# Kernel optimization log

Hardware: AMD Instinct MI355X
Metric: run time of the kernel (lower is better)

## Reference

```python
import jax, jax.numpy as jnp
import numpy as np

B, N, C, H = 4, 4096, 128, 4


def setup_inputs() -> dict:
    key = jax.random.key(0)
    ks = jax.random.split(key, 12)
    def rn(k, shape, s=0.02):
        return jax.random.normal(k, shape, jnp.float32) * s
    return dict(
        x=jax.random.normal(ks[0], (B, N, C), jnp.float32),
        p=jax.random.normal(ks[1], (B, N, 3), jnp.float32),
        fcl1_w=rn(ks[2], (C, C)), fcl1_b=jnp.zeros((C,), jnp.float32),
        # per-head (stacked over leading H axis) TransformerLayer params
        hq_w=rn(ks[3], (H, C, C)), hq_b=jnp.zeros((H, C), jnp.float32),
        hk_w=rn(ks[4], (H, C, C)), hk_b=jnp.zeros((H, C), jnp.float32),
        hv_w=rn(ks[5], (H, C, C)), hv_b=jnp.zeros((H, C), jnp.float32),
        pe1_w=rn(ks[6], (H, C, 3)), pe1_b=jnp.zeros((H, C), jnp.float32),  # Conv1d(3->C, k=1)
        pe2_w=rn(ks[7], (H, C, C)), pe2_b=jnp.zeros((H, C), jnp.float32),  # Conv1d(C->C, k=1)
        mh_w=rn(ks[8], (C, 4 * C)), mh_b=jnp.zeros((C,), jnp.float32),
        fcl2_w=rn(ks[9], (C, C)), fcl2_b=jnp.zeros((C,), jnp.float32),
    )


def reference(x, p, fcl1_w, fcl1_b, hq_w, hq_b, hk_w, hk_b, hv_w, hv_b,
              pe1_w, pe1_b, pe2_w, pe2_b, mh_w, mh_b, fcl2_w, fcl2_b):
    residual = x
    xf = x @ fcl1_w.T + fcl1_b  # fcl1
    scale = 1.0 / jnp.sqrt(jnp.asarray(C, jnp.float32))

    def head(qw, qb, kw, kb, vw, vb, p1w, p1b, p2w, p2b):
        # kernel-size-1 Conv1d == pointwise linear over coords
        pe = jax.nn.relu(jnp.einsum('bnd,cd->bnc', p, p1w) + p1b)
        pe = jnp.einsum('bnc,dc->bnd', pe, p2w) + p2b
        xh = xf + pe
        q = xh @ kw.T + kb  # note: original uses self.key for x_query
        k = xh @ qw.T + qb  # and self.query for x_key (name swap, kept faithful)
        v = xh @ vw.T + vb
        s = jax.nn.softmax(jnp.einsum('bnc,bmc->bnm', q, k) * scale, axis=-1)
        return jnp.einsum('bnm,bmc->bnc', s, v)

    outs = jax.vmap(head)(hq_w, hq_b, hk_w, hk_b, hv_w, hv_b,
                          pe1_w, pe1_b, pe2_w, pe2_b)  # [H,B,N,C]
    cat = jnp.moveaxis(outs, 0, 2).reshape(B, N, H * C)  # concat head1..head4 on last dim
    y = cat @ mh_w.T + mh_b
    y = y @ fcl2_w.T + fcl2_b
    mu = jnp.mean(y, axis=-1, keepdims=True)
    var = jnp.var(y, axis=-1, keepdims=True)
    y = (y - mu) / jnp.sqrt(var + 1e-5)  # torch.layer_norm, no affine
    return (y + residual, p)
```

## Files before the change

### kernel.cpp

```cpp
#include <hip/hip_runtime.h>
#include <hip/hip_bf16.h>

typedef __bf16 bf16;
typedef bf16 bf16x8 __attribute__((ext_vector_type(8)));
typedef float f32x4 __attribute__((ext_vector_type(4)));

static __device__ __forceinline__ f32x4 mfma16(bf16x8 a, bf16x8 b, f32x4 c) {
  return __builtin_amdgcn_mfma_f32_16x16x32_bf16(a, b, c, 0, 0, 0);
}

typedef __attribute__((address_space(3))) void lds_t;
typedef const __attribute__((address_space(1))) void gm_t;

#define N_SEG 18
#define TOTAL_CONV 2511616

struct ConvArgs { const void* src[N_SEG]; };

__global__ __launch_bounds__(256) void convall_k(ConvArgs a, bf16* __restrict__ dst,
                                                 void* __restrict__ outp,
                                                 int* __restrict__ flag) {
  const int ends[N_SEG] = {2097152, 2146304, 2162688, 2162816, 2228352, 2228864,
                           2294400, 2294912, 2360448, 2360960, 2362496, 2363008,
                           2428544, 2429056, 2494592, 2495104, 2511488, 2511616};
  const unsigned short* xr = (const unsigned short*)a.src[0];
  int wild = 0;
#pragma unroll
  for (int j = 0; j < 2; j++) {
    unsigned short w = xr[threadIdx.x * 2 + j];
    int e = (w >> 7) & 0xFF;
    if (e < 110 || e > 134) wild++;
  }
#pragma unroll
  for (int off = 1; off < 64; off <<= 1) wild += __shfl_xor(wild, off);
  __shared__ int red[4];
  if ((threadIdx.x & 63) == 0) red[threadIdx.x >> 6] = wild;
  __syncthreads();
  const int isF32 = (red[0] + red[1] + red[2] + red[3]) > 64;
  if (blockIdx.x == 0 && threadIdx.x == 0) *flag = isF32;

  int i = blockIdx.x * 256 + threadIdx.x;
  if (i >= TOTAL_CONV) {
    int j = i - TOTAL_CONV;
    if (j < 49152) {
      if (isF32) ((float*)outp)[2097152 + j] = ((const float*)a.src[1])[j];
      else       ((bf16*)outp)[2097152 + j]  = ((const bf16*)a.src[1])[j];
    }
    return;
  }
  int s = 0;
  while (i >= ends[s]) s++;
  int j = i - (s ? ends[s - 1] : 0);
  if (isF32) dst[i] = (bf16)((const float*)a.src[s])[j];
  else       dst[i] = ((const bf16*)a.src[s])[j];
}

__global__ __launch_bounds__(256, 2) void pre_k(
    const bf16* __restrict__ x, const bf16* __restrict__ p,
    const bf16* __restrict__ f1w, const bf16* __restrict__ f1b,
    const bf16* __restrict__ pe1w, const bf16* __restrict__ pe1b,
    const bf16* __restrict__ pe2w, const bf16* __restrict__ pe2b,
    const bf16* __restrict__ Wq, const bf16* __restrict__ Bq,
    const bf16* __restrict__ Wk, const bf16* __restrict__ Bk,
    const bf16* __restrict__ Wv, const bf16* __restrict__ Bv,
    bf16* __restrict__ qo, bf16* __restrict__ ko, bf16* __restrict__ vo)
{
  const int lane = threadIdx.x & 63;
  const int wave = threadIdx.x >> 6;
  const int quad = lane >> 4;
  const int n15 = lane & 15;
  const int h = blockIdx.y;
  const int r0 = blockIdx.x * 64;
  const int wr = wave * 16;

  __shared__ bf16 tile[9216];

  f32x4 acc[8];
  const f32x4 zz = {};

  {
    bf16x8 ap = {};
    if (quad == 0) {
      const bf16* pr = p + (long)(r0 + wr + n15) * 3;
      ap[0] = pr[0]; ap[1] = pr[1]; ap[2] = pr[2];
    }
#pragma unroll
    for (int ct = 0; ct < 8; ct++) {
      bf16x8 bw = {};
      if (quad == 0) {
        const bf16* wp = pe1w + ((long)h * 128 + ct * 16 + n15) * 3;
        bw[0] = wp[0]; bw[1] = wp[1]; bw[2] = wp[2];
      }
      acc[ct] = mfma16(ap, bw, zz);
    }
#pragma unroll
    for (int ct = 0; ct < 8; ct++) {
      const int col = ct * 16 + n15;
      const float bb = (float)pe1b[h * 128 + col];
#pragma unroll
      for (int r = 0; r < 4; r++)
        tile[(wr + quad * 4 + r) * 136 + col] = (bf16)fmaxf(acc[ct][r] + bb, 0.f);
    }
  }

#pragma unroll
  for (int ct = 0; ct < 8; ct++) acc[ct] = zz;
#pragma unroll
  for (int kk = 0; kk < 4; kk++) {
    const int ka = kk * 32 + quad * 8;
    bf16x8 a0 = *(const bf16x8*)&tile[(wr + n15) * 136 + ka];
#pragma unroll
    for (int ct = 0; ct < 8; ct++) {
      bf16x8 wf = *(const bf16x8*)(pe2w + (long)h * 16384 + (long)(ct * 16 + n15) * 128 + ka);
      acc[ct] = mfma16(a0, wf, acc[ct]);
    }
  }
#pragma unroll
  for (int kk = 0; kk < 4; kk++) {
    const int ka = kk * 32 + quad * 8;
    bf16x8 a0 = *(const bf16x8*)(x + (long)(r0 + wr + n15) * 128 + ka);
#pragma unroll
    for (int ct = 0; ct < 8; ct++) {
      bf16x8 wf = *(const bf16x8*)(f1w + (long)(ct * 16 + n15) * 128 + ka);
      acc[ct] = mfma16(a0, wf, acc[ct]);
    }
  }
#pragma unroll
  for (int ct = 0; ct < 8; ct++) {
    const int col = ct * 16 + n15;
    const float bv = (float)pe2b[h * 128 + col] + (float)f1b[col];
#pragma unroll
    for (int r = 0; r < 4; r++)
      tile[(wr + quad * 4 + r) * 136 + col] = (bf16)(acc[ct][r] + bv);
  }

  bf16x8 af[4];
#pragma unroll
  for (int kk = 0; kk < 4; kk++)
    af[kk] = *(const bf16x8*)&tile[(wr + n15) * 136 + kk * 32 + quad * 8];

#pragma unroll
  for (int m = 0; m < 2; m++) {
    f32x4 a2[8];
#pragma unroll
    for (int ct = 0; ct < 8; ct++) a2[ct] = zz;
    const bf16* Wm = (m == 0) ? Wq : Wk;
#pragma unroll
    for (int kk = 0; kk < 4; kk++) {
      const int ka = kk * 32 + quad * 8;
#pragma unroll
      for (int ct = 0; ct < 8; ct++) {
        bf16x8 wf = *(const bf16x8*)(Wm + (long)h * 16384 + (long)(ct * 16 + n15) * 128 + ka);
        a2[ct] = mfma16(af[kk], wf, a2[ct]);
      }
    }
    bf16* oz = ((m == 0) ? qo : ko) + (long)h * 2097152;
    const bf16* Bz = (m == 0) ? Bq : Bk;
    const float sc = (m == 0) ? 0.12751743f : 1.0f;
#pragma unroll
    for (int ct = 0; ct < 8; ct++) {
      const int col = ct * 16 + n15;
      const float bv = (float)Bz[h * 128 + col];
#pragma unroll
      for (int r = 0; r < 4; r++)
        oz[(long)(r0 + wr + quad * 4 + r) * 128 + col] = (bf16)((a2[ct][r] + bv) * sc);
    }
  }

  {
    f32x4 a2[8];
#pragma unroll
    for (int ct = 0; ct < 8; ct++) a2[ct] = zz;
#pragma unroll
    for (int kk = 0; kk < 4; kk++) {
      const int ka = kk * 32 + quad * 8;
#pragma unroll
      for (int ct = 0; ct < 8; ct++) {
        bf16x8 wf = *(const bf16x8*)(Wv + (long)h * 16384 + (long)(ct * 16 + n15) * 128 + ka);
        a2[ct] = mfma16(af[kk], wf, a2[ct]);
      }
    }
    __syncthreads();
#pragma unroll
    for (int ct = 0; ct < 8; ct++) {
      const int col = ct * 16 + n15;
      const float bv = (float)Bv[h * 128 + col];
#pragma unroll
      for (int r = 0; r < 4; r++)
        tile[col * 72 + (wr + quad * 4 + r)] = (bf16)(a2[ct][r] + bv);
    }
    __syncthreads();
    bf16* vz = vo + (long)h * 2097152;
#pragma unroll
    for (int i = 0; i < 16; i++) {
      const int c = wave * 32 + i * 2 + (lane >> 5);
      const int m2 = (lane & 31) * 2;
      *(unsigned int*)&vz[(long)c * 16384 + r0 + m2] =
          *(const unsigned int*)&tile[c * 72 + m2];
    }
  }
}

__global__ __launch_bounds__(256, 2) void attn_k(
    const bf16* __restrict__ Q, const bf16* __restrict__ Kg,
    const bf16* __restrict__ vT, bf16* __restrict__ cat)
{
  const int lane = threadIdx.x & 63;
  const int wave = threadIdx.x >> 6;
  const int quad = lane >> 4;
  const int n15 = lane & 15;
  const int b = blockIdx.y, h = blockIdx.z;
  const long qkBase = ((long)h * 4 + b) * 4096 * 128;
  const long vBase = (long)h * (128L * 16384) + (long)b * 4096;
  const int wrow = blockIdx.x * 128 + wave * 32;

  __shared__ bf16 Kt[2][64 * 128];
  __shared__ bf16 Vt[2][128 * 64];
  __shared__ bf16 Pt[8][1024];

  bf16x8 qf[2][4];
#pragma unroll
  for (int g = 0; g < 2; g++)
#pragma unroll
    for (int kk = 0; kk < 4; kk++)
      qf[g][kk] = *(const bf16x8*)(Q + qkBase + (long)(wrow + g * 16 + n15) * 128 + kk * 32 + quad * 8);

  const int krl  = lane >> 4;
  const int kpch = lane & 15;
  const int vcl  = lane >> 3;
  const int vpch = lane & 7;

  f32x4 Om[2][8] = {};
  float l_part[2][4] = {};

#pragma unroll
  for (int i = 0; i < 4; i++) {
    const int row = wave * 16 + i * 4 + krl;
    const int ch = kpch ^ (row & 15);
    __builtin_amdgcn_global_load_lds(
        (gm_t*)(Kg + qkBase + (long)row * 128 + ch * 8),
        (lds_t*)&Kt[0][(wave * 16 + i * 4) * 128], 16, 0, 0);
  }
#pragma unroll
  for (int i = 0; i < 4; i++) {
    const int c = wave * 32 + i * 8 + vcl;
    const int vch = vpch ^ (c & 7);
    __builtin_amdgcn_global_load_lds(
        (gm_t*)(vT + vBase + (long)c * 16384 + vch * 8),
        (lds_t*)&Vt[0][(wave * 32 + i * 8) * 64], 16, 0, 0);
  }

  for (int it = 0; it < 64; it++) {
    __syncthreads();
    const int cb = it & 1;
    if (it + 1 < 64) {
      const int kv1 = (it + 1) * 64;
      const int nb = cb ^ 1;
#pragma unroll
      for (int i = 0; i < 4; i++) {
        const int row = wave * 16 + i * 4 + krl;
        const int ch = kpch ^ (row & 15);
        __builtin_amdgcn_global_load_lds(
            (gm_t*)(Kg + qkBase + (long)(kv1 + row) * 128 + ch * 8),
            (lds_t*)&Kt[nb][(wave * 16 + i * 4) * 128], 16, 0, 0);
      }
#pragma unroll
      for (int i = 0; i < 4; i++) {
        const int c = wave * 32 + i * 8 + vcl;
        const int vch = vpch ^ (c & 7);
        __builtin_amdgcn_global_load_lds(
            (gm_t*)(vT + vBase + (long)c * 16384 + kv1 + vch * 8),
            (lds_t*)&Vt[nb][(wave * 32 + i * 8) * 64], 16, 0, 0);
      }
    }

    f32x4 S[2][4] = {};
#pragma unroll
    for (int kk = 0; kk < 4; kk++) {
#pragma unroll
      for (int ct = 0; ct < 4; ct++) {
        bf16x8 kf = *(const bf16x8*)&Kt[cb][(ct * 16 + n15) * 128 + (((kk * 4 + quad) ^ n15) * 8)];
        S[0][ct] = mfma16(qf[0][kk], kf, S[0][ct]);
        S[1][ct] = mfma16(qf[1][kk], kf, S[1][ct]);
      }
    }

#pragma unroll
    for (int g = 0; g < 2; g++)
#pragma unroll
      for (int ct = 0; ct < 4; ct++)
#pragma unroll
        for (int r = 0; r < 4; r++) {
          float e = __builtin_amdgcn_exp2f(S[g][ct][r]);
          l_part[g][r] += e;
          const int row = quad * 4 + r;
          const int kv = ct * 16 + n15;
          Pt[wave * 2 + g][row * 64 + ((((kv >> 3) ^ (row & 7)) * 8)) + (kv & 7)] = (bf16)e;
        }

#pragma unroll
    for (int kk = 0; kk < 2; kk++) {
      bf16x8 vf[8];
#pragma unroll
      for (int ct = 0; ct < 8; ct++) {
        const int c = ct * 16 + n15;
        vf[ct] = *(const bf16x8*)&Vt[cb][c * 64 + (((kk * 4 + quad) ^ (c & 7)) * 8)];
      }
#pragma unroll
      for (int g = 0; g < 2; g++) {
        bf16x8 pf = *(const bf16x8*)&Pt[wave * 2 + g][n15 * 64 + (((kk * 4 + quad) ^ (n15 & 7)) * 8)];
#pragma unroll
        for (int ct = 0; ct < 8; ct++)
          Om[g][ct] = mfma16(pf, vf[ct], Om[g][ct]);
      }
    }
  }

#pragma unroll
  for (int g = 0; g < 2; g++) {
    float inv[4];
#pragma unroll
    for (int r = 0; r < 4; r++) {
      float s = l_part[g][r];
#pragma unroll
      for (int off = 1; off < 16; off <<= 1) s += __shfl_xor(s, off);
      inv[r] = 1.f / s;
    }
    const long ob = ((long)b * 4096 + wrow + g * 16 + quad * 4) * 512 + h * 128;
#pragma unroll
    for (int ct = 0; ct < 8; ct++)
#pragma unroll
      for (int r = 0; r < 4; r++)
        cat[ob + (long)r * 512 + ct * 16 + n15] = (bf16)(Om[g][ct][r] * inv[r]);
  }
}

__global__ __launch_bounds__(256) void tail_k(
    const bf16* __restrict__ cat,
    const bf16* __restrict__ mhw, const bf16* __restrict__ mhb,
    const bf16* __restrict__ f2w, const bf16* __restrict__ f2b,
    const void* __restrict__ xraw, void* __restrict__ outraw,
    const int* __restrict__ flag)
{
  const int lane = threadIdx.x & 63;
  const int wave = threadIdx.x >> 6;
  const int quad = lane >> 4;
  const int n15 = lane & 15;
  const int r0 = blockIdx.x * 64 + wave * 16;
  __shared__ bf16 y1t[64][136];

  f32x4 acc[8] = {};
  for (int k0 = 0; k0 < 512; k0 += 32) {
    const int ka = k0 + quad * 8;
    bf16x8 a0 = *(const bf16x8*)(cat + (long)(r0 + n15) * 512 + ka);
#pragma unroll
    for (int ct = 0; ct < 8; ct++) {
      bf16x8 wf = *(const bf16x8*)(mhw + (long)(ct * 16 + n15) * 512 + ka);
      acc[ct] = mfma16(a0, wf, acc[ct]);
    }
  }
#pragma unroll
  for (int ct = 0; ct < 8; ct++) {
    const float bv = (float)mhb[ct * 16 + n15];
#pragma unroll
    for (int r = 0; r < 4; r++)
      y1t[wave * 16 + quad * 4 + r][ct * 16 + n15] = (bf16)(acc[ct][r] + bv);
  }

  f32x4 acc2[8] = {};
  for (int k0 = 0; k0 < 128; k0 += 32) {
    const int ka = k0 + quad * 8;
    bf16x8 a0 = *(const bf16x8*)&y1t[wave * 16 + n15][ka];
#pragma unroll
    for (int ct = 0; ct < 8; ct++) {
      bf16x8 wf = *(const bf16x8*)(f2w + (long)(ct * 16 + n15) * 128 + ka);
      acc2[ct] = mfma16(a0, wf, acc2[ct]);
    }
  }

  float s1[4] = {}, s2[4] = {};
#pragma unroll
  for (int ct = 0; ct < 8; ct++) {
    const float bv = (float)f2b[ct * 16 + n15];
#pragma unroll
    for (int r = 0; r < 4; r++) {
      const float v = acc2[ct][r] + bv;
      acc2[ct][r] = v;
      s1[r] += v;
      s2[r] += v * v;
    }
  }
  float mu[4], inv[4];
#pragma unroll
  for (int r = 0; r < 4; r++) {
    float a = s1[r], b2 = s2[r];
#pragma unroll
    for (int off = 1; off < 16; off <<= 1) {
      a += __shfl_xor(a, off);
      b2 += __shfl_xor(b2, off);
    }
    mu[r] = a * (1.f / 128.f);
    const float var = fmaxf(b2 * (1.f / 128.f) - mu[r] * mu[r], 0.f);
    inv[r] = rsqrtf(var + 1e-5f);
  }

  const int isF32 = *flag;
#pragma unroll
  for (int ct = 0; ct < 8; ct++)
#pragma unroll
    for (int r = 0; r < 4; r++) {
      const long idx = (long)(r0 + quad * 4 + r) * 128 + ct * 16 + n15;
      const float resid = isF32 ? ((const float*)xraw)[idx]
                                : (float)((const bf16*)xraw)[idx];
      const float v = (acc2[ct][r] - mu[r]) * inv[r] + resid;
      if (isF32) ((float*)outraw)[idx] = v;
      else       ((bf16*)outraw)[idx] = (bf16)v;
    }
}

extern "C" void kernel_launch(void* const* d_in, const int* in_sizes, int n_in,
                              void* d_out, int out_size, void* d_ws, size_t ws_size,
                              hipStream_t stream)
{
  bf16* ws  = (bf16*)d_ws;
  bf16* q   = ws;
  bf16* kb  = ws + 8388608;
  bf16* vt  = ws + 16777216;
  bf16* cat = ws + 25165824;
  const long AR = 33554432;
  int* flag = (int*)(ws + 36066048);

  static const int counts[N_SEG] = {2097152, 49152, 16384, 128, 65536, 512, 65536, 512,
                                    65536, 512, 1536, 512, 65536, 512, 65536, 512, 16384, 128};
  long offs[N_SEG]; long o = AR;
  for (int i = 0; i < N_SEG; i++) { offs[i] = o; o += counts[i]; }
  bf16* xc    = ws + offs[0];
  bf16* pc    = ws + offs[1];
  bf16* f1w   = ws + offs[2];
  bf16* f1b   = ws + offs[3];
  bf16* hqw   = ws + offs[4];
  bf16* hqb   = ws + offs[5];
  bf16* hkw   = ws + offs[6];
  bf16* hkb   = ws + offs[7];
  bf16* hvw   = ws + offs[8];
  bf16* hvb   = ws + offs[9];
  bf16* pe1w  = ws + offs[10];
  bf16* pe1b  = ws + offs[11];
  bf16* pe2w  = ws + offs[12];
  bf16* pe2b  = ws + offs[13];
  bf16* mhw   = ws + offs[14];
  bf16* mhb   = ws + offs[15];
  bf16* f2w   = ws + offs[16];
  bf16* f2b   = ws + offs[17];

  ConvArgs ca;
  for (int i = 0; i < N_SEG; i++) ca.src[i] = d_in[i];
  convall_k<<<dim3((TOTAL_CONV + 49152 + 255) / 256), dim3(256), 0, stream>>>(ca, ws + AR, d_out, flag);

  dim3 blk(256);
  pre_k<<<dim3(256, 4), blk, 0, stream>>>(xc, pc, f1w, f1b, pe1w, pe1b, pe2w, pe2b,
                                          hkw, hkb, hqw, hqb, hvw, hvb, q, kb, vt);
  attn_k<<<dim3(32, 4, 4), blk, 0, stream>>>(q, kb, vt, cat);
  tail_k<<<dim3(256), blk, 0, stream>>>(cat, mhw, mhb, f2w, f2b, d_in[0], d_out, flag);
}
```

Before: 358.2 us.

## Vectorize conversion, double rows per wave in pre_k, split tail_k columns across waves

The conversion kernel now handles 8 elements per thread with vector loads and stores. pre_k gives each wave 32 rows instead of 16, so every weight fragment feeds two MFMAs, and it writes the transposed V with 16-byte stores. tail_k shrinks to 16 rows per 128-thread block, with the two waves splitting the output columns and combining layernorm sums through shared memory, which yields four times as many blocks. The risks are more register pressure in pre_k, fewer pre_k blocks, and an extra barrier in tail_k. Segment boundaries in the conversion must be multiples of 8, which they appear to be.

```diff
diff --git a/kernel.cpp b/kernel.cpp
--- a/kernel.cpp
+++ b/kernel.cpp
@@ -39,20 +39,31 @@
   const int isF32 = (red[0] + red[1] + red[2] + red[3]) > 64;
   if (blockIdx.x == 0 && threadIdx.x == 0) *flag = isF32;
 
-  int i = blockIdx.x * 256 + threadIdx.x;
+  long i = ((long)blockIdx.x * 256 + threadIdx.x) * 8;
   if (i >= TOTAL_CONV) {
-    int j = i - TOTAL_CONV;
+    long j = i - TOTAL_CONV;
     if (j < 49152) {
-      if (isF32) ((float*)outp)[2097152 + j] = ((const float*)a.src[1])[j];
-      else       ((bf16*)outp)[2097152 + j]  = ((const bf16*)a.src[1])[j];
+      if (isF32) {
+#pragma unroll
+        for (int t = 0; t < 8; t++)
+          ((float*)outp)[2097152 + j + t] = ((const float*)a.src[1])[j + t];
+      } else {
+        *(bf16x8*)&((bf16*)outp)[2097152 + j] = *(const bf16x8*)&((const bf16*)a.src[1])[j];
+      }
     }
     return;
   }
   int s = 0;
   while (i >= ends[s]) s++;
-  int j = i - (s ? ends[s - 1] : 0);
-  if (isF32) dst[i] = (bf16)((const float*)a.src[s])[j];
-  else       dst[i] = ((const bf16*)a.src[s])[j];
+  long j = i - (s ? ends[s - 1] : 0);
+  if (isF32) {
+    bf16x8 v;
+#pragma unroll
+    for (int t = 0; t < 8; t++) v[t] = (bf16)((const float*)a.src[s])[j + t];
+    *(bf16x8*)&dst[i] = v;
+  } else {
+    *(bf16x8*)&dst[i] = *(const bf16x8*)&((const bf16*)a.src[s])[j];
+  }
 }
 
 __global__ __launch_bounds__(256, 2) void pre_k(
@@ -70,19 +81,21 @@
   const int quad = lane >> 4;
   const int n15 = lane & 15;
   const int h = blockIdx.y;
-  const int r0 = blockIdx.x * 64;
-  const int wr = wave * 16;
-
-  __shared__ bf16 tile[9216];
-
-  f32x4 acc[8];
+  const int r0 = blockIdx.x * 128;
+  const int wr = wave * 32;
+
+  __shared__ bf16 tile[128 * 136];
+
+  f32x4 acc[2][8];
   const f32x4 zz = {};
 
   {
-    bf16x8 ap = {};
+    bf16x8 ap0 = {}, ap1 = {};
     if (quad == 0) {
-      const bf16* pr = p + (long)(r0 + wr + n15) * 3;
-      ap[0] = pr[0]; ap[1] = pr[1]; ap[2] = pr[2];
+      const bf16* pr0 = p + (long)(r0 + wr + n15) * 3;
+      const bf16* pr1 = p + (long)(r0 + wr + 16 + n15) * 3;
+      ap0[0] = pr0[0]; ap0[1] = pr0[1]; ap0[2] = pr0[2];
+      ap1[0] = pr1[0]; ap1[1] = pr1[1]; ap1[2] = pr1[2];
     }
 #pragma unroll
     for (int ct = 0; ct < 8; ct++) {
@@ -91,59 +104,73 @@
         const bf16* wp = pe1w + ((long)h * 128 + ct * 16 + n15) * 3;
         bw[0] = wp[0]; bw[1] = wp[1]; bw[2] = wp[2];
       }
-      acc[ct] = mfma16(ap, bw, zz);
-    }
-#pragma unroll
-    for (int ct = 0; ct < 8; ct++) {
-      const int col = ct * 16 + n15;
-      const float bb = (float)pe1b[h * 128 + col];
-#pragma unroll
-      for (int r = 0; r < 4; r++)
-        tile[(wr + quad * 4 + r) * 136 + col] = (bf16)fmaxf(acc[ct][r] + bb, 0.f);
-    }
-  }
-
-#pragma unroll
-  for (int ct = 0; ct < 8; ct++) acc[ct] = zz;
+      acc[0][ct] = mfma16(ap0, bw, zz);
+      acc[1][ct] = mfma16(ap1, bw, zz);
+    }
+#pragma unroll
+    for (int g = 0; g < 2; g++)
+#pragma unroll
+      for (int ct = 0; ct < 8; ct++) {
+        const int col = ct * 16 + n15;
+        const float bb = (float)pe1b[h * 128 + col];
+#pragma unroll
+        for (int r = 0; r < 4; r++)
+          tile[(wr + g * 16 + quad * 4 + r) * 136 + col] = (bf16)fmaxf(acc[g][ct][r] + bb, 0.f);
+      }
+  }
+
+#pragma unroll
+  for (int g = 0; g < 2; g++)
+#pragma unroll
+    for (int ct = 0; ct < 8; ct++) acc[g][ct] = zz;
 #pragma unroll
   for (int kk = 0; kk < 4; kk++) {
     const int ka = kk * 32 + quad * 8;
     bf16x8 a0 = *(const bf16x8*)&tile[(wr + n15) * 136 + ka];
+    bf16x8 a1 = *(const bf16x8*)&tile[(wr + 16 + n15) * 136 + ka];
 #pragma unroll
     for (int ct = 0; ct < 8; ct++) {
       bf16x8 wf = *(const bf16x8*)(pe2w + (long)h * 16384 + (long)(ct * 16 + n15) * 128 + ka);
-      acc[ct] = mfma16(a0, wf, acc[ct]);
+      acc[0][ct] = mfma16(a0, wf, acc[0][ct]);
+      acc[1][ct] = mfma16(a1, wf, acc[1][ct]);
     }
   }
 #pragma unroll
   for (int kk = 0; kk < 4; kk++) {
     const int ka = kk * 32 + quad * 8;
     bf16x8 a0 = *(const bf16x8*)(x + (long)(r0 + wr + n15) * 128 + ka);
+    bf16x8 a1 = *(const bf16x8*)(x + (long)(r0 + wr + 16 + n15) * 128 + ka);
 #pragma unroll
     for (int ct = 0; ct < 8; ct++) {
       bf16x8 wf = *(const bf16x8*)(f1w + (long)(ct * 16 + n15) * 128 + ka);
-      acc[ct] = mfma16(a0, wf, acc[ct]);
-    }
-  }
-#pragma unroll
-  for (int ct = 0; ct < 8; ct++) {
-    const int col = ct * 16 + n15;
-    const float bv = (float)pe2b[h * 128 + col] + (float)f1b[col];
-#pragma unroll
-    for (int r = 0; r < 4; r++)
-      tile[(wr + quad * 4 + r) * 136 + col] = (bf16)(acc[ct][r] + bv);
-  }
-
-  bf16x8 af[4];
-#pragma unroll
-  for (int kk = 0; kk < 4; kk++)
-    af[kk] = *(const bf16x8*)&tile[(wr + n15) * 136 + kk * 32 + quad * 8];
+      acc[0][ct] = mfma16(a0, wf, acc[0][ct]);
+      acc[1][ct] = mfma16(a1, wf, acc[1][ct]);
+    }
+  }
+#pragma unroll
+  for (int g = 0; g < 2; g++)
+#pragma unroll
+    for (int ct = 0; ct < 8; ct++) {
+      const int col = ct * 16 + n15;
+      const float bv = (float)pe2b[h * 128 + col] + (float)f1b[col];
+#pragma unroll
+      for (int r = 0; r < 4; r++)
+        tile[(wr + g * 16 + quad * 4 + r) * 136 + col] = (bf16)(acc[g][ct][r] + bv);
+    }
+
+  bf16x8 af[2][4];
+#pragma unroll
+  for (int g = 0; g < 2; g++)
+#pragma unroll
+    for (int kk = 0; kk < 4; kk++)
+      af[g][kk] = *(const bf16x8*)&tile[(wr + g * 16 + n15) * 136 + kk * 32 + quad * 8];
 
 #pragma unroll
   for (int m = 0; m < 2; m++) {
-    f32x4 a2[8];
-#pragma unroll
-    for (int ct = 0; ct < 8; ct++) a2[ct] = zz;
+#pragma unroll
+    for (int g = 0; g < 2; g++)
+#pragma unroll
+      for (int ct = 0; ct < 8; ct++) acc[g][ct] = zz;
     const bf16* Wm = (m == 0) ? Wq : Wk;
 #pragma unroll
     for (int kk = 0; kk < 4; kk++) {
@@ -151,52 +178,59 @@
 #pragma unroll
       for (int ct = 0; ct < 8; ct++) {
         bf16x8 wf = *(const bf16x8*)(Wm + (long)h * 16384 + (long)(ct * 16 + n15) * 128 + ka);
-        a2[ct] = mfma16(af[kk], wf, a2[ct]);
+        acc[0][ct] = mfma16(af[0][kk], wf, acc[0][ct]);
+        acc[1][ct] = mfma16(af[1][kk], wf, acc[1][ct]);
       }
     }
     bf16* oz = ((m == 0) ? qo : ko) + (long)h * 2097152;
     const bf16* Bz = (m == 0) ? Bq : Bk;
     const float sc = (m == 0) ? 0.12751743f : 1.0f;
 #pragma unroll
-    for (int ct = 0; ct < 8; ct++) {
-      const int col = ct * 16 + n15;
-      const float bv = (float)Bz[h * 128 + col];
-#pragma unroll
-      for (int r = 0; r < 4; r++)
-        oz[(long)(r0 + wr + quad * 4 + r) * 128 + col] = (bf16)((a2[ct][r] + bv) * sc);
-    }
+    for (int g = 0; g < 2; g++)
+#pragma unroll
+      for (int ct = 0; ct < 8; ct++) {
+        const int col = ct * 16 + n15;
+        const float bv = (float)Bz[h * 128 + col];
+#pragma unroll
+        for (int r = 0; r < 4; r++)
+          oz[(long)(r0 + wr + g * 16 + quad * 4 + r) * 128 + col] = (bf16)((acc[g][ct][r] + bv) * sc);
+      }
   }
 
   {
-    f32x4 a2[8];
-#pragma unroll
-    for (int ct = 0; ct < 8; ct++) a2[ct] = zz;
+#pragma unroll
+    for (int g = 0; g < 2; g++)
+#pragma unroll
+      for (int ct = 0; ct < 8; ct++) acc[g][ct] = zz;
 #pragma unroll
     for (int kk = 0; kk < 4; kk++) {
       const int ka = kk * 32 + quad * 8;
 #pragma unroll
       for (int ct = 0; ct < 8; ct++) {
         bf16x8 wf = *(const bf16x8*)(Wv + (long)h * 16384 + (long)(ct * 16 + n15) * 128 + ka);
-        a2[ct] = mfma16(af[kk], wf, a2[ct]);
+        acc[0][ct] = mfma16(af[0][kk], wf, acc[0][ct]);
+        acc[1][ct] = mfma16(af[1][kk], wf, acc[1][ct]);
       }
     }
     __syncthreads();
 #pragma unroll
-    for (int ct = 0; ct < 8; ct++) {
-      const int col = ct * 16 + n15;
-      const float bv = (float)Bv[h * 128 + col];
-#pragma unroll
-      for (int r = 0; r < 4; r++)
-        tile[col * 72 + (wr + quad * 4 + r)] = (bf16)(a2[ct][r] + bv);
-    }
+    for (int g = 0; g < 2; g++)
+#pragma unroll
+      for (int ct = 0; ct < 8; ct++) {
+        const int col = ct * 16 + n15;
+        const float bv = (float)Bv[h * 128 + col];
+#pragma unroll
+        for (int r = 0; r < 4; r++)
+          tile[col * 136 + (wr + g * 16 + quad * 4 + r)] = (bf16)(acc[g][ct][r] + bv);
+      }
     __syncthreads();
     bf16* vz = vo + (long)h * 2097152;
-#pragma unroll
-    for (int i = 0; i < 16; i++) {
-      const int c = wave * 32 + i * 2 + (lane >> 5);
-      const int m2 = (lane & 31) * 2;
-      *(unsigned int*)&vz[(long)c * 16384 + r0 + m2] =
-          *(const unsigned int*)&tile[c * 72 + m2];
+    const int mloc = (threadIdx.x & 15) * 8;
+    const int cbase = threadIdx.x >> 4;
+#pragma unroll
+    for (int cc = 0; cc < 8; cc++) {
+      const int c = cc * 16 + cbase;
+      *(bf16x8*)&vz[(long)c * 16384 + r0 + mloc] = *(const bf16x8*)&tile[c * 136 + mloc];
     }
   }
 }
@@ -335,7 +369,7 @@
   }
 }
 
-__global__ __launch_bounds__(256) void tail_k(
+__global__ __launch_bounds__(128) void tail_k(
     const bf16* __restrict__ cat,
     const bf16* __restrict__ mhw, const bf16* __restrict__ mhb,
     const bf16* __restrict__ f2w, const bf16* __restrict__ f2b,
@@ -346,42 +380,45 @@
   const int wave = threadIdx.x >> 6;
   const int quad = lane >> 4;
   const int n15 = lane & 15;
-  const int r0 = blockIdx.x * 64 + wave * 16;
-  __shared__ bf16 y1t[64][136];
-
-  f32x4 acc[8] = {};
+  const int r0 = blockIdx.x * 16;
+  __shared__ bf16 y1t[16][136];
+  __shared__ float lred[2][2][16];
+
+  f32x4 acc[4] = {};
   for (int k0 = 0; k0 < 512; k0 += 32) {
     const int ka = k0 + quad * 8;
     bf16x8 a0 = *(const bf16x8*)(cat + (long)(r0 + n15) * 512 + ka);
 #pragma unroll
-    for (int ct = 0; ct < 8; ct++) {
-      bf16x8 wf = *(const bf16x8*)(mhw + (long)(ct * 16 + n15) * 512 + ka);
+    for (int ct = 0; ct < 4; ct++) {
+      bf16x8 wf = *(const bf16x8*)(mhw + (long)(wave * 64 + ct * 16 + n15) * 512 + ka);
       acc[ct] = mfma16(a0, wf, acc[ct]);
     }
   }
 #pragma unroll
-  for (int ct = 0; ct < 8; ct++) {
-    const float bv = (float)mhb[ct * 16 + n15];
+  for (int ct = 0; ct < 4; ct++) {
+    const int col = wave * 64 + ct * 16 + n15;
+    const float bv = (float)mhb[col];
 #pragma unroll
     for (int r = 0; r < 4; r++)
-      y1t[wave * 16 + quad * 4 + r][ct * 16 + n15] = (bf16)(acc[ct][r] + bv);
-  }
-
-  f32x4 acc2[8] = {};
+      y1t[quad * 4 + r][col] = (bf16)(acc[ct][r] + bv);
+  }
+  __syncthreads();
+
+  f32x4 acc2[4] = {};
   for (int k0 = 0; k0 < 128; k0 += 32) {
     const int ka = k0 + quad * 8;
-    bf16x8 a0 = *(const bf16x8*)&y1t[wave * 16 + n15][ka];
-#pragma unroll
-    for (int ct = 0; ct < 8; ct++) {
-      bf16x8 wf = *(const bf16x8*)(f2w + (long)(ct * 16 + n15) * 128 + ka);
+    bf16x8 a0 = *(const bf16x8*)&y1t[n15][ka];
+#pragma unroll
+    for (int ct = 0; ct < 4; ct++) {
+      bf16x8 wf = *(const bf16x8*)(f2w + (long)(wave * 64 + ct * 16 + n15) * 128 + ka);
       acc2[ct] = mfma16(a0, wf, acc2[ct]);
     }
   }
 
   float s1[4] = {}, s2[4] = {};
 #pragma unroll
-  for (int ct = 0; ct < 8; ct++) {
-    const float bv = (float)f2b[ct * 16 + n15];
+  for (int ct = 0; ct < 4; ct++) {
+    const float bv = (float)f2b[wave * 64 + ct * 16 + n15];
 #pragma unroll
     for (int r = 0; r < 4; r++) {
       const float v = acc2[ct][r] + bv;
@@ -390,7 +427,6 @@
       s2[r] += v * v;
     }
   }
-  float mu[4], inv[4];
 #pragma unroll
   for (int r = 0; r < 4; r++) {
     float a = s1[r], b2 = s2[r];
@@ -399,23 +435,29 @@
       a += __shfl_xor(a, off);
       b2 += __shfl_xor(b2, off);
     }
-    mu[r] = a * (1.f / 128.f);
-    const float var = fmaxf(b2 * (1.f / 128.f) - mu[r] * mu[r], 0.f);
-    inv[r] = rsqrtf(var + 1e-5f);
-  }
+    if (n15 == 0) { lred[wave][0][quad * 4 + r] = a; lred[wave][1][quad * 4 + r] = b2; }
+  }
+  __syncthreads();
 
   const int isF32 = *flag;
 #pragma unroll
-  for (int ct = 0; ct < 8; ct++)
-#pragma unroll
-    for (int r = 0; r < 4; r++) {
-      const long idx = (long)(r0 + quad * 4 + r) * 128 + ct * 16 + n15;
+  for (int r = 0; r < 4; r++) {
+    const int row = quad * 4 + r;
+    const float tot = lred[0][0][row] + lred[1][0][row];
+    const float tot2 = lred[0][1][row] + lred[1][1][row];
+    const float mu = tot * (1.f / 128.f);
+    const float var = fmaxf(tot2 * (1.f / 128.f) - mu * mu, 0.f);
+    const float inv = rsqrtf(var + 1e-5f);
+#pragma unroll
+    for (int ct = 0; ct < 4; ct++) {
+      const long idx = (long)(r0 + row) * 128 + wave * 64 + ct * 16 + n15;
       const float resid = isF32 ? ((const float*)xraw)[idx]
                                 : (float)((const bf16*)xraw)[idx];
-      const float v = (acc2[ct][r] - mu[r]) * inv[r] + resid;
+      const float v = (acc2[ct][r] - mu) * inv + resid;
       if (isF32) ((float*)outraw)[idx] = v;
       else       ((bf16*)outraw)[idx] = (bf16)v;
     }
+  }
 }
 
 extern "C" void kernel_launch(void* const* d_in, const int* in_sizes, int n_in,
@@ -455,11 +497,10 @@
 
   ConvArgs ca;
   for (int i = 0; i < N_SEG; i++) ca.src[i] = d_in[i];
-  convall_k<<<dim3((TOTAL_CONV + 49152 + 255) / 256), dim3(256), 0, stream>>>(ca, ws + AR, d_out, flag);
-
-  dim3 blk(256);
-  pre_k<<<dim3(256, 4), blk, 0, stream>>>(xc, pc, f1w, f1b, pe1w, pe1b, pe2w, pe2b,
-                                          hkw, hkb, hqw, hqb, hvw, hvb, q, kb, vt);
-  attn_k<<<dim3(32, 4, 4), blk, 0, stream>>>(q, kb, vt, cat);
-  tail_k<<<dim3(256), blk, 0, stream>>>(cat, mhw, mhb, f2w, f2b, d_in[0], d_out, flag);
+  convall_k<<<dim3((TOTAL_CONV + 49152 + 2047) / 2048), dim3(256), 0, stream>>>(ca, ws + AR, d_out, flag);
+
+  pre_k<<<dim3(128, 4), dim3(256), 0, stream>>>(xc, pc, f1w, f1b, pe1w, pe1b, pe2w, pe2b,
+                                                hkw, hkb, hqw, hqb, hvw, hvb, q, kb, vt);
+  attn_k<<<dim3(32, 4, 4), dim3(256), 0, stream>>>(q, kb, vt, cat);
+  tail_k<<<dim3(1024), dim3(128), 0, stream>>>(cat, mhw, mhb, f2w, f2b, d_in[0], d_out, flag);
 }
```

Result: faster. 328.6 us (-8.3%).
